# Optimization experiments

Hardware: AMD Instinct MI355X
Metric: run time of the kernel (lower is better)

Reference implementation:

```python
import jax, jax.numpy as jnp
import numpy as np

N = 40000
IN_DIM = 128
HID = 64
E = 640000


def sage_conv(x, edge_index, W_l, b_l, W_r):
    """PyG SAGEConv with mean aggregation.
    out = lin_l(mean_{j in N(i)} x_j) + lin_r(x_i)
    edge_index[0]=src (message source), edge_index[1]=dst (aggregation target).
    """
    src, dst = edge_index[0], edge_index[1]
    n = x.shape[0]
    msgs = x[src]                                            # [E, d] gather
    sums = jax.ops.segment_sum(msgs, dst, num_segments=n)    # [N, d]
    cnt = jax.ops.segment_sum(jnp.ones((msgs.shape[0],), x.dtype), dst,
                              num_segments=n)                # [N]
    mean = sums / jnp.maximum(cnt, 1.0)[:, None]
    return mean @ W_l.T + b_l + x @ W_r.T


def setup_inputs() -> dict:
    key = jax.random.key(0)
    ks = jax.random.split(key, 8)
    x = jax.random.normal(ks[0], (N, IN_DIM), dtype=jnp.float32)
    edge_index = jax.random.randint(ks[1], (2, E), 0, N, dtype=jnp.int32)
    s1 = 1.0 / np.sqrt(IN_DIM)
    s2 = 1.0 / np.sqrt(HID)
    W1_l = jax.random.uniform(ks[2], (HID, IN_DIM), jnp.float32, -s1, s1)
    b1_l = jax.random.uniform(ks[3], (HID,), jnp.float32, -s1, s1)
    W1_r = jax.random.uniform(ks[4], (HID, IN_DIM), jnp.float32, -s1, s1)
    W2_l = jax.random.uniform(ks[5], (HID, HID), jnp.float32, -s2, s2)
    b2_l = jax.random.uniform(ks[6], (HID,), jnp.float32, -s2, s2)
    W2_r = jax.random.uniform(ks[7], (HID, HID), jnp.float32, -s2, s2)
    return {"x": x, "edge_index": edge_index,
            "W1_l": W1_l, "b1_l": b1_l, "W1_r": W1_r,
            "W2_l": W2_l, "b2_l": b2_l, "W2_r": W2_r}


def reference(x, edge_index, W1_l, b1_l, W1_r, W2_l, b2_l, W2_r):
    h = sage_conv(x, edge_index, W1_l, b1_l, W1_r)
    h = jax.nn.relu(h)
    # dropout is identity in eval mode (reference baseline is deterministic)
    z = sage_conv(h, edge_index, W2_l, b2_l, W2_r)
    return z
```

## Files before the change

### kernel.cpp

```cpp
#include <hip/hip_runtime.h>

#define INDIM 128
#define HID 64
#define CAP 64
#define GEMM_BLOCKS 625
#define SCAT_BLOCKS 1875
#define CNTS 5

__device__ __forceinline__ float bf2f(unsigned short u) {
    union { unsigned int i; float f; } c; c.i = ((unsigned int)u) << 16; return c.f;
}
__device__ __forceinline__ unsigned short f2bf(float f) {
    union { float f; unsigned int i; } c; c.f = f;
    return (unsigned short)((c.i + 0x7FFFu + ((c.i >> 16) & 1u)) >> 16);
}

__device__ __forceinline__ float4 gather4(const unsigned short* __restrict__ Pb,
                                          int row, int f4) {
    const uint2 v = *(const uint2*)&Pb[(size_t)row * 64 + f4 * 4];
    float4 r;
    r.x = bf2f((unsigned short)(v.x & 0xffffu));
    r.y = bf2f((unsigned short)(v.x >> 16));
    r.z = bf2f((unsigned short)(v.y & 0xffffu));
    r.w = bf2f((unsigned short)(v.y >> 16));
    return r;
}

__device__ __forceinline__ float4 agg_core(const unsigned short* __restrict__ Pb,
                                           int idx0, int deg, int q, int f4) {
    float4 acc = make_float4(0.f, 0.f, 0.f, 0.f);
    const int nchunk = (deg + 3) >> 2;
    for (int c = 0; c < nchunk; c += 4) {
        #pragma unroll
        for (int u = 0; u < 4; ++u) {
            const int cc = c + u;
            const int lanesel = cc * 4 + q;
            const int sidx = __shfl(idx0, lanesel, 64);
            const float m = (cc < nchunk && lanesel < deg) ? 1.f : 0.f;
            const float4 v = gather4(Pb, sidx, f4);
            acc.x += v.x * m; acc.y += v.y * m;
            acc.z += v.z * m; acc.w += v.w * m;
        }
    }
    acc.x += __shfl_xor(acc.x, 16, 64); acc.y += __shfl_xor(acc.y, 16, 64);
    acc.z += __shfl_xor(acc.z, 16, 64); acc.w += __shfl_xor(acc.w, 16, 64);
    acc.x += __shfl_xor(acc.x, 32, 64); acc.y += __shfl_xor(acc.y, 32, 64);
    acc.z += __shfl_xor(acc.z, 32, 64); acc.w += __shfl_xor(acc.w, 32, 64);
    return acc;
}


__global__ __launch_bounds__(256) void k_prep(
    const float* __restrict__ W1l, const float* __restrict__ W1r,
    const float* __restrict__ W2l, const float* __restrict__ W2r,
    float* __restrict__ WT1l, float* __restrict__ WT1r,
    float* __restrict__ WT2l, float* __restrict__ WT2r,
    int* __restrict__ cnt, int n) {
    int gtid = blockIdx.x * 256 + threadIdx.x;
    if (gtid < n) cnt[gtid << CNTS] = 0;
    if (gtid < 64 * 128) {
        int j = gtid >> 7, k = gtid & 127;
        WT1l[k * 64 + j] = W1l[gtid];
        WT1r[k * 64 + j] = W1r[gtid];
    }
    if (gtid < 64 * 64) {
        int j = gtid >> 6, k = gtid & 63;
        WT2l[k * 64 + j] = W2l[gtid];
        WT2r[k * 64 + j] = W2r[gtid];
    }
}


__global__ __launch_bounds__(256) void k_gemm1_scatter(
    const float* __restrict__ A,
    const float* __restrict__ WTl, const float* __restrict__ WTr,
    unsigned short* __restrict__ Pb, float* __restrict__ Q,
    const int* __restrict__ src, const int* __restrict__ dst,
    int* __restrict__ cnt, unsigned short* __restrict__ sorted, int N, int E) {
    __shared__ float As[64][INDIM + 1];
    const int tid = threadIdx.x;

    if (blockIdx.x >= GEMM_BLOCKS) {
        const int b = blockIdx.x - GEMM_BLOCKS;
        const int stride = SCAT_BLOCKS * 256;
        for (int e = b * 256 + tid; e < E; e += stride) {
            const int d = dst[e];
            const int slot = atomicAdd(&cnt[d << CNTS], 1);
            if (slot < CAP) sorted[(d << 6) + slot] = (unsigned short)src[e];
        }
        return;
    }

    const int bm = blockIdx.x * 64;
    for (int idx = tid; idx < 64 * 32; idx += 256) {
        int row = idx >> 5, kq = idx & 31;
        const float4 v = ((const float4*)A)[(size_t)(bm + row) * 32 + kq];
        As[row][kq * 4 + 0] = v.x; As[row][kq * 4 + 1] = v.y;
        As[row][kq * 4 + 2] = v.z; As[row][kq * 4 + 3] = v.w;
    }
    __syncthreads();

    const int tx = tid & 15, ty = tid >> 4;
    const int n0 = ty * 4;
    float accl[4][4] = {}, accr[4][4] = {};
    #pragma unroll 8
    for (int k = 0; k < INDIM; ++k) {
        float a[4];
        #pragma unroll
        for (int i = 0; i < 4; ++i) a[i] = As[n0 + i][k];
        const float4 blv = ((const float4*)WTl)[k * 16 + tx];
        const float4 brv = ((const float4*)WTr)[k * 16 + tx];
        const float bl[4] = {blv.x, blv.y, blv.z, blv.w};
        const float br[4] = {brv.x, brv.y, brv.z, brv.w};
        #pragma unroll
        for (int i = 0; i < 4; ++i) {
            #pragma unroll
            for (int j = 0; j < 4; ++j) {
                accl[i][j] += a[i] * bl[j];
                accr[i][j] += a[i] * br[j];
            }
        }
    }
    #pragma unroll
    for (int i = 0; i < 4; ++i) {
        int m = bm + n0 + i;
        ushort4 pv;
        pv.x = f2bf(accl[i][0]); pv.y = f2bf(accl[i][1]);
        pv.z = f2bf(accl[i][2]); pv.w = f2bf(accl[i][3]);
        ((ushort4*)Pb)[(size_t)m * 16 + tx] = pv;
        ((float4*)Q)[(size_t)m * 16 + tx] =
            make_float4(accr[i][0], accr[i][1], accr[i][2], accr[i][3]);
    }
}


__global__ __launch_bounds__(256) void k_agg1(
    const unsigned short* __restrict__ Pb, const float* __restrict__ Q,
    const float* __restrict__ b1,
    const int* __restrict__ cnt, const unsigned short* __restrict__ sorted,
    float* __restrict__ H, int N) {
    const int wid  = (blockIdx.x * 256 + threadIdx.x) >> 6;
    const int lane = threadIdx.x & 63;
    const int q = lane >> 4, f4 = lane & 15;
    if (wid >= N) return;
    int deg = cnt[wid << CNTS]; if (deg > CAP) deg = CAP;
    const int ls = (lane < deg) ? lane : ((deg > 0) ? deg - 1 : 0);
    const int idx0 = (deg > 0) ? (int)sorted[(wid << 6) + ls] : 0;
    const float4 a = agg_core(Pb, idx0, deg, q, f4);
    if (q == 0) {
        const float inv = 1.0f / fmaxf((float)deg, 1.0f);
        const float4 qv = *(const float4*)&Q[(size_t)wid * 64 + f4 * 4];
        const float4 bv = *(const float4*)&b1[f4 * 4];
        float4 hv;
        hv.x = fmaxf(a.x * inv + bv.x + qv.x, 0.f);
        hv.y = fmaxf(a.y * inv + bv.y + qv.y, 0.f);
        hv.z = fmaxf(a.z * inv + bv.z + qv.z, 0.f);
        hv.w = fmaxf(a.w * inv + bv.w + qv.w, 0.f);
        *(float4*)&H[(size_t)wid * 64 + f4 * 4] = hv;
    }
}


__global__ __launch_bounds__(256) void k_gemm2(
    const float* __restrict__ H,
    const float* __restrict__ WTl, const float* __restrict__ WTr,
    unsigned short* __restrict__ Pb2, float* __restrict__ Q2, int N) {
    __shared__ float As[64][HID + 1];
    const int tid = threadIdx.x;
    const int bm = blockIdx.x * 64;
    for (int idx = tid; idx < 64 * 16; idx += 256) {
        int row = idx >> 4, kq = idx & 15;
        const float4 v = ((const float4*)H)[(size_t)(bm + row) * 16 + kq];
        As[row][kq * 4 + 0] = v.x; As[row][kq * 4 + 1] = v.y;
        As[row][kq * 4 + 2] = v.z; As[row][kq * 4 + 3] = v.w;
    }
    __syncthreads();

    const int tx = tid & 15, ty = tid >> 4;
    const int n0 = ty * 4;
    float accl[4][4] = {}, accr[4][4] = {};
    #pragma unroll 8
    for (int k = 0; k < HID; ++k) {
        float a[4];
        #pragma unroll
        for (int i = 0; i < 4; ++i) a[i] = As[n0 + i][k];
        const float4 blv = ((const float4*)WTl)[k * 16 + tx];
        const float4 brv = ((const float4*)WTr)[k * 16 + tx];
        const float bl[4] = {blv.x, blv.y, blv.z, blv.w};
        const float br[4] = {brv.x, brv.y, brv.z, brv.w};
        #pragma unroll
        for (int i = 0; i < 4; ++i) {
            #pragma unroll
            for (int j = 0; j < 4; ++j) {
                accl[i][j] += a[i] * bl[j];
                accr[i][j] += a[i] * br[j];
            }
        }
    }
    #pragma unroll
    for (int i = 0; i < 4; ++i) {
        int m = bm + n0 + i;
        if (m < N) {
            ushort4 pv;
            pv.x = f2bf(accl[i][0]); pv.y = f2bf(accl[i][1]);
            pv.z = f2bf(accl[i][2]); pv.w = f2bf(accl[i][3]);
            ((ushort4*)Pb2)[(size_t)m * 16 + tx] = pv;
            ((float4*)Q2)[(size_t)m * 16 + tx] =
                make_float4(accr[i][0], accr[i][1], accr[i][2], accr[i][3]);
        }
    }
}


__global__ __launch_bounds__(256) void k_agg2(
    const unsigned short* __restrict__ Pb2, const float* __restrict__ Q2,
    const float* __restrict__ b2,
    const int* __restrict__ cnt, const unsigned short* __restrict__ sorted,
    float* __restrict__ z, int N) {
    const int wid  = (blockIdx.x * 256 + threadIdx.x) >> 6;
    const int lane = threadIdx.x & 63;
    const int q = lane >> 4, f4 = lane & 15;
    if (wid >= N) return;
    int deg = cnt[wid << CNTS]; if (deg > CAP) deg = CAP;
    const int ls = (lane < deg) ? lane : ((deg > 0) ? deg - 1 : 0);
    const int idx0 = (deg > 0) ? (int)sorted[(wid << 6) + ls] : 0;
    const float4 a = agg_core(Pb2, idx0, deg, q, f4);
    if (q == 0) {
        const float inv = 1.0f / fmaxf((float)deg, 1.0f);
        const float4 qv = *(const float4*)&Q2[(size_t)wid * 64 + f4 * 4];
        const float4 bv = *(const float4*)&b2[f4 * 4];
        float4 zv;
        zv.x = a.x * inv + bv.x + qv.x;
        zv.y = a.y * inv + bv.y + qv.y;
        zv.z = a.z * inv + bv.z + qv.z;
        zv.w = a.w * inv + bv.w + qv.w;
        *(float4*)&z[(size_t)wid * 64 + f4 * 4] = zv;
    }
}


extern "C" void kernel_launch(void* const* d_in, const int* in_sizes, int n_in,
                              void* d_out, int out_size, void* d_ws, size_t ws_size,
                              hipStream_t stream) {
    const float* x   = (const float*)d_in[0];
    const int*  edge = (const int*)d_in[1];
    const float* W1l = (const float*)d_in[2];
    const float* b1l = (const float*)d_in[3];
    const float* W1r = (const float*)d_in[4];
    const float* W2l = (const float*)d_in[5];
    const float* b2l = (const float*)d_in[6];
    const float* W2r = (const float*)d_in[7];

    const int N = in_sizes[0] / INDIM;
    const int E = in_sizes[1] / 2;
    const int* src = edge;
    const int* dst = edge + E;

    char* w = (char*)d_ws;
    auto carve = [&](size_t bytes) {
        char* p = w; w += (bytes + 255) & ~(size_t)255; return p;
    };
    unsigned short* Pb  = (unsigned short*)carve((size_t)N * 64 * 2);
    float* Q    = (float*)carve((size_t)N * 64 * 4);
    float* H    = (float*)carve((size_t)N * 64 * 4);
    float* WT1l = (float*)carve(128 * 64 * 4);
    float* WT1r = (float*)carve(128 * 64 * 4);
    float* WT2l = (float*)carve(64 * 64 * 4);
    float* WT2r = (float*)carve(64 * 64 * 4);
    int* cnt    = (int*)carve((size_t)N * (4 << CNTS));
    unsigned short* sorted = (unsigned short*)carve((size_t)N * CAP * 2);

    float* zout = (float*)d_out;

    const int gT = (N + 63) / 64;
    const int gN = (N + 255) / 256;
    const int gW = (N * 64 + 255) / 256;

    k_prep<<<gN, 256, 0, stream>>>(W1l, W1r, W2l, W2r,
                                   WT1l, WT1r, WT2l, WT2r, cnt, N);
    k_gemm1_scatter<<<GEMM_BLOCKS + SCAT_BLOCKS, 256, 0, stream>>>(
        x, WT1l, WT1r, Pb, Q, src, dst, cnt, sorted, N, E);
    k_agg1<<<gW, 256, 0, stream>>>(Pb, Q, b1l, cnt, sorted, H, N);
    k_gemm2<<<gT, 256, 0, stream>>>(H, WT2l, WT2r, Pb, Q, N);
    k_agg2<<<gW, 256, 0, stream>>>(Pb, Q, b2l, cnt, sorted, zout, N);
}
```

Before: 118.4 us.

## Replace global-atomic edge scatter with two-pass range binning and shared-memory placement

Replaces the per-edge global atomicAdd scatter into padded per-node counters with a two-pass bucket sort. A block-local histogram over 128-node ranges reserves space in global bins, and a new k_place kernel fills the per-node neighbor lists using shared-memory atomics. The aim is to cut the cost of heavy global atomic traffic and of the padded counter array. It adds an extra kernel launch and an intermediate packed edge buffer. It also adds a fixed per-bin capacity that silently drops edges if a range overflows it.

```diff
diff --git a/kernel.cpp b/kernel.cpp
--- a/kernel.cpp
+++ b/kernel.cpp
@@ -4,8 +4,11 @@
 #define HID 64
 #define CAP 64
 #define GEMM_BLOCKS 625
-#define SCAT_BLOCKS 1875
-#define CNTS 5
+#define BIN_BLOCKS 64
+#define RSH 7
+#define RMASK ((1 << RSH) - 1)
+#define NRANGE 313
+#define BINCAP 2560
 
 __device__ __forceinline__ float bf2f(unsigned short u) {
     union { unsigned int i; float f; } c; c.i = ((unsigned int)u) << 16; return c.f;
@@ -55,9 +58,9 @@
     const float* __restrict__ W2l, const float* __restrict__ W2r,
     float* __restrict__ WT1l, float* __restrict__ WT1r,
     float* __restrict__ WT2l, float* __restrict__ WT2r,
-    int* __restrict__ cnt, int n) {
+    unsigned int* __restrict__ bin_cnt) {
     int gtid = blockIdx.x * 256 + threadIdx.x;
-    if (gtid < n) cnt[gtid << CNTS] = 0;
+    if (gtid < NRANGE) bin_cnt[gtid] = 0;
     if (gtid < 64 * 128) {
         int j = gtid >> 7, k = gtid & 127;
         WT1l[k * 64 + j] = W1l[gtid];
@@ -71,22 +74,39 @@
 }
 
 
-__global__ __launch_bounds__(256) void k_gemm1_scatter(
+__global__ __launch_bounds__(256) void k_gemm1_bin(
     const float* __restrict__ A,
     const float* __restrict__ WTl, const float* __restrict__ WTr,
     unsigned short* __restrict__ Pb, float* __restrict__ Q,
     const int* __restrict__ src, const int* __restrict__ dst,
-    int* __restrict__ cnt, unsigned short* __restrict__ sorted, int N, int E) {
+    unsigned int* __restrict__ bin_cnt, unsigned int* __restrict__ ebin,
+    int N, int E) {
     __shared__ float As[64][INDIM + 1];
+    __shared__ unsigned int hist[NRANGE];
+    __shared__ unsigned int cur[NRANGE];
     const int tid = threadIdx.x;
 
     if (blockIdx.x >= GEMM_BLOCKS) {
         const int b = blockIdx.x - GEMM_BLOCKS;
-        const int stride = SCAT_BLOCKS * 256;
-        for (int e = b * 256 + tid; e < E; e += stride) {
-            const int d = dst[e];
-            const int slot = atomicAdd(&cnt[d << CNTS], 1);
-            if (slot < CAP) sorted[(d << 6) + slot] = (unsigned short)src[e];
+        const int ech = (E + BIN_BLOCKS - 1) / BIN_BLOCKS;
+        const int e0 = b * ech;
+        const int e1 = (e0 + ech < E) ? e0 + ech : E;
+        for (int r = tid; r < NRANGE; r += 256) hist[r] = 0;
+        __syncthreads();
+        for (int e = e0 + tid; e < e1; e += 256)
+            atomicAdd(&hist[((unsigned)dst[e]) >> RSH], 1u);
+        __syncthreads();
+        for (int r = tid; r < NRANGE; r += 256) {
+            const unsigned c = hist[r];
+            cur[r] = c ? atomicAdd(&bin_cnt[r], c) : 0u;
+        }
+        __syncthreads();
+        for (int e = e0 + tid; e < e1; e += 256) {
+            const unsigned d = (unsigned)dst[e];
+            const unsigned s = (unsigned)src[e];
+            const unsigned r = d >> RSH;
+            const unsigned off = atomicAdd(&cur[r], 1u);
+            if (off < BINCAP) ebin[(size_t)r * BINCAP + off] = (d << 16) | s;
         }
         return;
     }
@@ -134,6 +154,32 @@
 }
 
 
+__global__ __launch_bounds__(256) void k_place(
+    const unsigned int* __restrict__ bin_cnt,
+    const unsigned int* __restrict__ ebin,
+    int* __restrict__ cnt, unsigned short* __restrict__ sorted, int N) {
+    __shared__ unsigned int lcnt[1 << RSH];
+    const int tid = threadIdx.x;
+    const int r = blockIdx.x;
+    for (int l = tid; l < (1 << RSH); l += 256) lcnt[l] = 0;
+    __syncthreads();
+    unsigned c = bin_cnt[r];
+    if (c > BINCAP) c = BINCAP;
+    const unsigned int* eb = ebin + (size_t)r * BINCAP;
+    for (unsigned i = tid; i < c; i += 256) {
+        const unsigned p = eb[i];
+        const unsigned d = p >> 16;
+        const unsigned slot = atomicAdd(&lcnt[d & RMASK], 1u);
+        if (slot < CAP) sorted[(d << 6) + slot] = (unsigned short)(p & 0xffffu);
+    }
+    __syncthreads();
+    for (int l = tid; l < (1 << RSH); l += 256) {
+        const int node = (r << RSH) + l;
+        if (node < N) cnt[node] = (int)lcnt[l];
+    }
+}
+
+
 __global__ __launch_bounds__(256) void k_agg1(
     const unsigned short* __restrict__ Pb, const float* __restrict__ Q,
     const float* __restrict__ b1,
@@ -143,7 +189,7 @@
     const int lane = threadIdx.x & 63;
     const int q = lane >> 4, f4 = lane & 15;
     if (wid >= N) return;
-    int deg = cnt[wid << CNTS]; if (deg > CAP) deg = CAP;
+    int deg = cnt[wid]; if (deg > CAP) deg = CAP;
     const int ls = (lane < deg) ? lane : ((deg > 0) ? deg - 1 : 0);
     const int idx0 = (deg > 0) ? (int)sorted[(wid << 6) + ls] : 0;
     const float4 a = agg_core(Pb, idx0, deg, q, f4);
@@ -221,7 +267,7 @@
     const int lane = threadIdx.x & 63;
     const int q = lane >> 4, f4 = lane & 15;
     if (wid >= N) return;
-    int deg = cnt[wid << CNTS]; if (deg > CAP) deg = CAP;
+    int deg = cnt[wid]; if (deg > CAP) deg = CAP;
     const int ls = (lane < deg) ? lane : ((deg > 0) ? deg - 1 : 0);
     const int idx0 = (deg > 0) ? (int)sorted[(wid << 6) + ls] : 0;
     const float4 a = agg_core(Pb2, idx0, deg, q, f4);
@@ -267,8 +313,10 @@
     float* WT1r = (float*)carve(128 * 64 * 4);
     float* WT2l = (float*)carve(64 * 64 * 4);
     float* WT2r = (float*)carve(64 * 64 * 4);
-    int* cnt    = (int*)carve((size_t)N * (4 << CNTS));
+    int* cnt    = (int*)carve((size_t)N * 4);
     unsigned short* sorted = (unsigned short*)carve((size_t)N * CAP * 2);
+    unsigned int* bin_cnt  = (unsigned int*)carve((size_t)NRANGE * 4);
+    unsigned int* ebin     = (unsigned int*)carve((size_t)NRANGE * BINCAP * 4);
 
     float* zout = (float*)d_out;
 
@@ -277,9 +325,10 @@
     const int gW = (N * 64 + 255) / 256;
 
     k_prep<<<gN, 256, 0, stream>>>(W1l, W1r, W2l, W2r,
-                                   WT1l, WT1r, WT2l, WT2r, cnt, N);
-    k_gemm1_scatter<<<GEMM_BLOCKS + SCAT_BLOCKS, 256, 0, stream>>>(
-        x, WT1l, WT1r, Pb, Q, src, dst, cnt, sorted, N, E);
+                                   WT1l, WT1r, WT2l, WT2r, bin_cnt);
+    k_gemm1_bin<<<GEMM_BLOCKS + BIN_BLOCKS, 256, 0, stream>>>(
+        x, WT1l, WT1r, Pb, Q, src, dst, bin_cnt, ebin, N, E);
+    k_place<<<NRANGE, 256, 0, stream>>>(bin_cnt, ebin, cnt, sorted, N);
     k_agg1<<<gW, 256, 0, stream>>>(Pb, Q, b1l, cnt, sorted, H, N);
     k_gemm2<<<gT, 256, 0, stream>>>(H, WT2l, WT2r, Pb, Q, N);
     k_agg2<<<gW, 256, 0, stream>>>(Pb, Q, b2l, cnt, sorted, zout, N);
```

Measured after the change: 129.6 us. 9.4% more time.
